# Performance work log

Hardware: AMD Instinct MI355X
Metric: run time of the kernel (lower is better)

The kernel has to match this reference:

```python
import jax, jax.numpy as jnp
import numpy as np

_EPS = 1e-5

def _ln(x, scale, shift):
    # Faithful to the module's custom layer norm: variance term is the SUM of
    # squared deviations over the feature dim (not the mean), and the affine is
    # scale * normed + shift with scale=b*, shift=s* (argument order as in source).
    m = jnp.mean(x, axis=-1, keepdims=True)
    d = x - m
    ssq = jnp.sum(d * d, axis=-1, keepdims=True)
    return scale * (d / jnp.sqrt(ssq + _EPS)) + shift


def setup_inputs() -> dict:
    key = jax.random.key(0)
    ks = jax.random.split(key, 12)
    B, T, I, H = 64, 512, 512, 512
    f32 = jnp.float32
    return {
        "x": jax.random.normal(ks[0], (B, T, I), f32),
        "hx": jax.random.normal(ks[1], (B, H), f32),
        "cx": jax.random.normal(ks[2], (B, H), f32),
        "Wi": jax.random.normal(ks[3], (4 * H, I), f32) / np.float32(np.sqrt(I)),
        "Wh": jax.random.normal(ks[4], (4 * H, H), f32) / np.float32(np.sqrt(H)),
        "bias": jax.random.normal(ks[5], (4 * H,), f32) * 0.1,
        "b1": jax.random.normal(ks[6], (4 * H,), f32) * 0.1,
        "b2": jax.random.normal(ks[7], (4 * H,), f32) * 0.1,
        "b3": jax.random.normal(ks[8], (H,), f32) * 0.1,
        "s1": 1.0 + jax.random.normal(ks[9], (4 * H,), f32) * 0.1,
        "s2": 1.0 + jax.random.normal(ks[10], (4 * H,), f32) * 0.1,
        "s3": 1.0 + jax.random.normal(ks[11], (H,), f32) * 0.1,
    }


def reference(x, hx, cx, Wi, Wh, bias, b1, b2, b3, s1, s2, s3):
    # x: [B, T, I] (batch_first). Work in time-major for the scan.
    xT = jnp.swapaxes(x, 0, 1)  # [T, B, I]
    # The input-projection layer norm has no cross-time dependency -> precompute.
    gi = _ln(jnp.einsum('tbi,gi->tbg', xT, Wi), b1, s1)  # [T, B, 4H]

    def step(carry, gi_t):
        h, c = carry
        gates = gi_t + _ln(h @ Wh.T, b2, s2) + bias  # [B, 4H]
        i, f, g, o = jnp.split(gates, 4, axis=-1)
        i = jax.nn.sigmoid(i)
        f = jax.nn.sigmoid(f)
        g = jnp.tanh(g)
        o = jax.nn.sigmoid(o)
        c_new = _ln(f * c + i * g, b3, s3)
        h_new = o * jnp.tanh(c_new)
        return (h_new, c_new), h_new

    (hy, cy), ys = jax.lax.scan(step, (hx, cx), gi)
    output = jnp.swapaxes(ys, 0, 1)  # back to [B, T, H]
    return output, hy, cy
```

## Files before the change

kernel.cpp:

```cpp
#include <hip/hip_runtime.h>
#include <cstdint>
#include <cstddef>


typedef float  f32x4 __attribute__((ext_vector_type(4)));
typedef __bf16 bf16x8 __attribute__((ext_vector_type(8)));
typedef unsigned int u32x4 __attribute__((ext_vector_type(4)));
typedef unsigned short u16x4 __attribute__((ext_vector_type(4)));

#define DEV __device__ __forceinline__

#define LD4_AGENT(dst, p) asm volatile("global_load_dwordx4 %0, %1, off sc1" : "=v"(dst) : "v"(p))
#define VM0_FENCE() do{ asm volatile("s_waitcnt vmcnt(0)" ::: "memory"); \
                        __builtin_amdgcn_sched_barrier(0); }while(0)

DEV unsigned short f2b(float f){
  unsigned int u = __builtin_bit_cast(unsigned int, f);
  unsigned int r = (u + 0x7FFFu + ((u >> 16) & 1u)) >> 16;
  return (unsigned short)r;
}
DEV float b2f(unsigned short s){
  unsigned int u = ((unsigned int)s) << 16;
  return __builtin_bit_cast(float, u);
}
DEV float tanh_fast(float x){
  const float e = __expf(2.f * x);
  return 1.f - 2.f * __builtin_amdgcn_rcpf(e + 1.f);
}
DEV float sigmoid_fast(float x){
  return __builtin_amdgcn_rcpf(1.f + __expf(-x));
}

__global__ __launch_bounds__(256) void conv_bf16(const float* __restrict__ src,
                                                 unsigned short* __restrict__ dst,
                                                 int n4){
  int i = blockIdx.x * 256 + threadIdx.x;
  if (i >= n4) return;
  f32x4 v = ((const f32x4*)src)[i];
  u16x4 o;
  #pragma unroll
  for (int j = 0; j < 4; ++j) o[j] = f2b(v[j]);
  ((u16x4*)dst)[i] = o;
}

__global__ __launch_bounds__(256, 2) void gemm_gi(const unsigned short* __restrict__ Xb,
                                                  const unsigned short* __restrict__ Wib,
                                                  unsigned short* __restrict__ Gp){
  __shared__ unsigned short As[128 * 48];
  __shared__ unsigned short Bs[128 * 48];
  const int tid = threadIdx.x;
  const int m0 = blockIdx.x * 128;
  const int n0 = blockIdx.y * 128;
  const int w = tid >> 6, lane = tid & 63;
  const int lr = lane & 15, lq = lane >> 4;
  const int wm = (w & 1) * 64, wn = (w >> 1) * 64;
  const int sr = tid >> 2;
  const int sc = (tid & 3) * 8;
  const unsigned short* gx = Xb + (size_t)(m0 + sr) * 512 + sc;
  const unsigned short* gw = Wib + (size_t)(n0 + sr) * 512 + sc;
  f32x4 acc[4][4] = {};
  for (int kb = 0; kb < 16; ++kb){
    u32x4 a0 = *(const u32x4*)(gx + kb * 32);
    u32x4 a1 = *(const u32x4*)(gx + 64 * 512 + kb * 32);
    u32x4 b0 = *(const u32x4*)(gw + kb * 32);
    u32x4 b1 = *(const u32x4*)(gw + 64 * 512 + kb * 32);
    __syncthreads();
    *(u32x4*)&As[sr * 48 + sc] = a0;
    *(u32x4*)&As[(sr + 64) * 48 + sc] = a1;
    *(u32x4*)&Bs[sr * 48 + sc] = b0;
    *(u32x4*)&Bs[(sr + 64) * 48 + sc] = b1;
    __syncthreads();
    bf16x8 af[4], bfv[4];
    #pragma unroll
    for (int mi = 0; mi < 4; ++mi) af[mi] = *(const bf16x8*)&As[(wm + mi * 16 + lr) * 48 + lq * 8];
    #pragma unroll
    for (int ni = 0; ni < 4; ++ni) bfv[ni] = *(const bf16x8*)&Bs[(wn + ni * 16 + lr) * 48 + lq * 8];
    #pragma unroll
    for (int mi = 0; mi < 4; ++mi)
      #pragma unroll
      for (int ni = 0; ni < 4; ++ni)
        acc[mi][ni] = __builtin_amdgcn_mfma_f32_16x16x32_bf16(af[mi], bfv[ni], acc[mi][ni], 0, 0, 0);
  }
  #pragma unroll
  for (int mi = 0; mi < 4; ++mi){
    const int rowb = m0 + wm + mi * 16 + lq * 4;
    #pragma unroll
    for (int ni = 0; ni < 4; ++ni){
      const int col = n0 + wn + ni * 16 + lr;
      #pragma unroll
      for (int r = 0; r < 4; ++r)
        Gp[(size_t)(rowb + r) * 2048 + col] = f2b(acc[mi][ni][r]);
    }
  }
}

__global__ __launch_bounds__(256) void ln_rows(unsigned short* __restrict__ G,
                                               const float* __restrict__ b1,
                                               const float* __restrict__ s1){
  const int row = blockIdx.x;
  const int tid = threadIdx.x;
  unsigned short* rp = G + (size_t)row * 2048 + tid * 8;
  u32x4 raw = *(const u32x4*)rp;
  float x[8];
  #pragma unroll
  for (int j = 0; j < 8; ++j){
    unsigned int word = raw[j >> 1];
    unsigned short us = (j & 1) ? (unsigned short)(word >> 16) : (unsigned short)(word & 0xFFFF);
    x[j] = b2f(us);
  }
  float s = 0.f, q = 0.f;
  #pragma unroll
  for (int j = 0; j < 8; ++j){ s += x[j]; q += x[j] * x[j]; }
  #pragma unroll
  for (int o = 1; o < 64; o <<= 1){ s += __shfl_xor(s, o); q += __shfl_xor(q, o); }
  __shared__ float ps[4][2];
  const int wv = tid >> 6;
  if ((tid & 63) == 0){ ps[wv][0] = s; ps[wv][1] = q; }
  __syncthreads();
  s = ps[0][0] + ps[1][0] + ps[2][0] + ps[3][0];
  q = ps[0][1] + ps[1][1] + ps[2][1] + ps[3][1];
  const float mu = s * (1.f / 2048.f);
  const float inv = rsqrtf((q - s * mu) + 1e-5f);
  const float* b1p = b1 + tid * 8;
  const float* s1p = s1 + tid * 8;
  u32x4 outw;
  #pragma unroll
  for (int j = 0; j < 4; ++j){
    float y0 = b1p[2 * j]     * ((x[2 * j]     - mu) * inv) + s1p[2 * j];
    float y1 = b1p[2 * j + 1] * ((x[2 * j + 1] - mu) * inv) + s1p[2 * j + 1];
    outw[j] = (unsigned int)f2b(y0) | ((unsigned int)f2b(y1) << 16);
  }
  *(u32x4*)rp = outw;
}

__global__ __launch_bounds__(512, 2) void lstm_rec(
    const unsigned short* __restrict__ Gi,
    const unsigned short* __restrict__ Whb,
    const float* __restrict__ bias,
    const float* __restrict__ b2, const float* __restrict__ s2,
    const float* __restrict__ b3, const float* __restrict__ s3,
    const float* __restrict__ hx,
    const float* __restrict__ cx,
    unsigned int* __restrict__ hbuf,
    unsigned long long* __restrict__ pF,
    unsigned long long* __restrict__ pA,
    unsigned long long* __restrict__ pCs,
    float* __restrict__ out){
  const int tid = threadIdx.x;
  const int tm = (blockIdx.x >> 1) & 3;
  const int ks = ((blockIdx.x >> 3) << 1) | (blockIdx.x & 1);
  const int w = tid >> 6;
  const int lane = tid & 63;
  const int lr = lane & 15, lq = lane >> 4;

  const int type = w >> 1;
  const int jloc = (w & 1) * 16 + lr;
  const int row_g = type * 512 + ks * 32 + jloc;
  const float b2r = b2[row_g];
  const float sbr = s2[row_g] + bias[row_g];

  bf16x8 bfr[16];
  {
    const unsigned short* wr = Whb + (size_t)row_g * 512 + lq * 8;
    #pragma unroll
    for (int kk = 0; kk < 16; ++kk) bfr[kk] = *(const bf16x8*)(wr + kk * 32);
  }

  const int cs = tid >> 5;
  const int cj = tid & 31;
  const int hcol = ks * 32 + cj;
  const int bidx = tm * 16 + cs;
  float c_val = cx[(size_t)bidx * 512 + hcol];
  const float b3j = b3[hcol], s3j = s3[hcol];

  const int psmp = 2 * w + (lane >> 5);
  const int pidx = lane & 31;
  const int pl_slice = (lane >> 1) & 15;
  const int pl_kind  = lane & 1;

  float b3c[16], s3c[16];
  #pragma unroll
  for (int q = 0; q < 4; ++q)
    #pragma unroll
    for (int j = 0; j < 4; ++j){
      const int c = 4 * pidx + 128 * q + j;
      b3c[4 * q + j] = b3[c];
      s3c[4 * q + j] = s3[c];
    }

  __shared__ unsigned short hlds[16 * 520];
  __shared__ float act[4][32][17];
  __shared__ float redA[8][16][2];
  __shared__ float stAl[16][2];

  float cc_own = 0.f, o_own = 0.f;

  for (int t = 0; t < 512; ++t){
    float giv[4];
    #pragma unroll
    for (int r = 0; r < 4; ++r){
      const int b = tm * 16 + lq * 4 + r;
      giv[r] = b2f(Gi[((size_t)b * 512 + t) * 2048 + row_g]);
    }

    if (t == 0){
      const float* hr = hx + (size_t)(tm * 16 + psmp) * 512;
      #pragma unroll
      for (int q = 0; q < 4; ++q){
        f32x4 hv4 = *(const f32x4*)(hr + 4 * pidx + 128 * q);
        unsigned long long pk = 0;
        #pragma unroll
        for (int j = 0; j < 4; ++j)
          pk |= (unsigned long long)f2b(hv4[j]) << (16 * j);
        *(unsigned long long*)&hlds[psmp * 520 + 4 * pidx + 128 * q] = pk;
      }
    } else {
      const unsigned int tg = (unsigned)t;
      const unsigned long long* fp = pF + (size_t)(t & 1) * 64 + tm * 16 + (lane & 15);
      const unsigned long long* sp =
          pCs + ((size_t)(t & 1) * 4 + tm) * 512 + pl_slice * 32 + psmp * 2 + pl_kind;
      unsigned long long sv;
      for (;;){
        unsigned long long fv = __hip_atomic_load(fp, __ATOMIC_RELAXED, __HIP_MEMORY_SCOPE_AGENT);
        sv = __hip_atomic_load(sp, __ATOMIC_RELAXED, __HIP_MEMORY_SCOPE_AGENT);
        bool ok = ((unsigned)fv == tg) & ((unsigned)(sv >> 32) == tg);
        if (__all((int)ok)) break;
        __builtin_amdgcn_s_sleep(1);
      }
      const unsigned int* hsrc =
          hbuf + (size_t)(t & 1) * 32768 + (size_t)(tm * 16 + psmp) * 512;
      u32x4 pay[4];
      #pragma unroll
      for (int q = 0; q < 4; ++q) LD4_AGENT(pay[q], hsrc + 4 * pidx + 128 * q);
      float pv = __builtin_bit_cast(float, (unsigned)sv);
      #pragma unroll
      for (int o = 2; o < 32; o <<= 1) pv += __shfl_xor(pv, o);
      const float ov = __shfl_xor(pv, 1);
      const float S = pl_kind ? ov : pv;
      const float Q = pl_kind ? pv : ov;
      const float mu = S * (1.f / 512.f);
      const float inv = rsqrtf((Q - S * mu) + 1e-5f);
      c_val = b3j * ((cc_own - mu) * inv) + s3j;
      const float h_self = o_own * tanh_fast(c_val);
      out[((size_t)bidx * 512 + (t - 1)) * 512 + hcol] = h_self;
      VM0_FENCE();
      #pragma unroll
      for (int q = 0; q < 4; ++q){
        unsigned long long pk = 0;
        #pragma unroll
        for (int j = 0; j < 4; ++j){
          const unsigned int v = pay[q][j];
          const float ccv = b2f((unsigned short)(v & 0xFFFF));
          const float oov = b2f((unsigned short)(v >> 16));
          const float h = oov * tanh_fast(b3c[4 * q + j] * ((ccv - mu) * inv) + s3c[4 * q + j]);
          pk |= (unsigned long long)f2b(h) << (16 * j);
        }
        *(unsigned long long*)&hlds[psmp * 520 + 4 * pidx + 128 * q] = pk;
      }
    }
    __syncthreads();

    f32x4 acc = {0.f, 0.f, 0.f, 0.f};
    #pragma unroll
    for (int kk = 0; kk < 16; ++kk){
      bf16x8 af = *(const bf16x8*)&hlds[lr * 520 + lq * 8 + kk * 32];
      acc = __builtin_amdgcn_mfma_f32_16x16x32_bf16(af, bfr[kk], acc, 0, 0, 0);
    }
    #pragma unroll
    for (int r = 0; r < 4; ++r){
      float s = acc[r], q = acc[r] * acc[r];
      #pragma unroll
      for (int o = 1; o < 16; o <<= 1){ s += __shfl_xor(s, o); q += __shfl_xor(q, o); }
      if (lr == 0){ redA[w][lq * 4 + r][0] = s; redA[w][lq * 4 + r][1] = q; }
    }
    __syncthreads();

    unsigned long long* slotA = pA + ((size_t)(t & 1) * 4 + tm) * 512;
    const unsigned int atag = (unsigned)(t + 1);
    if (w == 0 && lane < 32){
      const int smp = lane >> 1, kd = lane & 1;
      float Sp = 0.f;
      #pragma unroll
      for (int w2 = 0; w2 < 8; ++w2) Sp += redA[w2][smp][kd];
      const unsigned long long pvs = ((unsigned long long)atag << 32) |
          (unsigned long long)__builtin_bit_cast(unsigned int, Sp);
      __hip_atomic_store(slotA + (size_t)ks * 32 + lane, pvs,
                         __ATOMIC_RELAXED, __HIP_MEMORY_SCOPE_AGENT);
    }
    {
      const unsigned long long* ap = slotA + pl_slice * 32 + psmp * 2 + pl_kind;
      unsigned long long av;
      for (;;){
        av = __hip_atomic_load(ap, __ATOMIC_RELAXED, __HIP_MEMORY_SCOPE_AGENT);
        if (__all((int)((unsigned)(av >> 32) == atag))) break;
        __builtin_amdgcn_s_sleep(2);
      }
      float pv = __builtin_bit_cast(float, (unsigned)av);
      #pragma unroll
      for (int o = 2; o < 32; o <<= 1) pv += __shfl_xor(pv, o);
      const float ov = __shfl_xor(pv, 1);
      const float S = pl_kind ? ov : pv;
      const float Q = pl_kind ? pv : ov;
      if ((lane & 31) == 0){
        const float mu = S * (1.f / 2048.f);
        stAl[psmp][0] = mu;
        stAl[psmp][1] = rsqrtf((Q - S * mu) + 1e-5f);
      }
    }
    __syncthreads();

    #pragma unroll
    for (int r = 0; r < 4; ++r){
      const int s0 = lq * 4 + r;
      const float nv = (acc[r] - stAl[s0][0]) * stAl[s0][1];
      const float gv = giv[r] + b2r * nv + sbr;
      float a;
      if (type == 2) a = tanh_fast(gv);
      else           a = sigmoid_fast(gv);
      act[type][jloc][s0] = a;
    }
    __syncthreads();

    const float i_g = act[0][cj][cs];
    const float f_g = act[1][cj][cs];
    const float g_g = act[2][cj][cs];
    const float o_g = act[3][cj][cs];
    const float cc = f_g * c_val + i_g * g_g;
    const unsigned int ntag = (unsigned)(t + 1);
    const size_t np = (size_t)((t + 1) & 1);
    {
      const unsigned int pv32 = (unsigned int)f2b(cc) | ((unsigned int)f2b(o_g) << 16);
      __hip_atomic_store(hbuf + np * 32768 + (size_t)bidx * 512 + hcol, pv32,
                         __ATOMIC_RELAXED, __HIP_MEMORY_SCOPE_AGENT);
    }
    float sC = cc, qC = cc * cc;
    #pragma unroll
    for (int o = 1; o < 32; o <<= 1){ sC += __shfl_xor(sC, o); qC += __shfl_xor(qC, o); }
    unsigned long long* slotC = pCs + (np * 4 + tm) * 512;
    if ((lane & 31) < 2){
      const float v = (lane & 1) ? qC : sC;
      const unsigned long long pvs = ((unsigned long long)ntag << 32) |
          (unsigned long long)__builtin_bit_cast(unsigned int, v);
      __hip_atomic_store(slotC + (size_t)ks * 32 + cs * 2 + (lane & 1), pvs,
                         __ATOMIC_RELAXED, __HIP_MEMORY_SCOPE_AGENT);
    }
    VM0_FENCE();
    __syncthreads();
    if (tid == 0)
      __hip_atomic_store(pF + np * 64 + tm * 16 + ks, (unsigned long long)ntag,
                         __ATOMIC_RELAXED, __HIP_MEMORY_SCOPE_AGENT);
    cc_own = cc; o_own = o_g;
  }

  {
    const unsigned long long* sp =
        pCs + ((size_t)0 * 4 + tm) * 512 + pl_slice * 32 + psmp * 2 + pl_kind;
    unsigned long long sv;
    for (;;){
      sv = __hip_atomic_load(sp, __ATOMIC_RELAXED, __HIP_MEMORY_SCOPE_AGENT);
      if (__all((int)((unsigned)(sv >> 32) == 512u))) break;
      __builtin_amdgcn_s_sleep(2);
    }
    float pv = __builtin_bit_cast(float, (unsigned)sv);
    #pragma unroll
    for (int o = 2; o < 32; o <<= 1) pv += __shfl_xor(pv, o);
    const float ov = __shfl_xor(pv, 1);
    const float S = pl_kind ? ov : pv;
    const float Q = pl_kind ? pv : ov;
    const float mu = S * (1.f / 512.f);
    const float inv = rsqrtf((Q - S * mu) + 1e-5f);
    const float cn = b3j * ((cc_own - mu) * inv) + s3j;
    const float h = o_own * tanh_fast(cn);
    out[((size_t)bidx * 512 + 511) * 512 + hcol] = h;
    out[16777216u + (size_t)bidx * 512 + hcol] = h;
    out[16777216u + 32768u + (size_t)bidx * 512 + hcol] = cn;
  }
}

extern "C" void kernel_launch(void* const* d_in, const int* in_sizes, int n_in,
                              void* d_out, int out_size, void* d_ws, size_t ws_size,
                              hipStream_t stream){
  (void)in_sizes; (void)n_in; (void)out_size; (void)ws_size;
  const float* x    = (const float*)d_in[0];
  const float* hx   = (const float*)d_in[1];
  const float* cx   = (const float*)d_in[2];
  const float* Wi   = (const float*)d_in[3];
  const float* Wh   = (const float*)d_in[4];
  const float* bias = (const float*)d_in[5];
  const float* b1   = (const float*)d_in[6];
  const float* b2   = (const float*)d_in[7];
  const float* b3   = (const float*)d_in[8];
  const float* s1   = (const float*)d_in[9];
  const float* s2   = (const float*)d_in[10];
  const float* s3   = (const float*)d_in[11];
  float* out = (float*)d_out;
  char* ws = (char*)d_ws;

  unsigned short*     xb   = (unsigned short*)(ws);
  unsigned short*     wib  = (unsigned short*)(ws + 33554432);
  unsigned short*     whb  = (unsigned short*)(ws + 35651584);
  unsigned short*     gp   = (unsigned short*)(ws + 37748736);
  unsigned int*       hbuf = (unsigned int*)(ws + 171966464);
  unsigned long long* pF   = (unsigned long long*)(ws + 172228608);
  unsigned long long* pA   = (unsigned long long*)(ws + 172490752);
  unsigned long long* pCs  = (unsigned long long*)(ws + 172523520);

  hipMemsetAsync(pF, 0, 327680, stream);
  conv_bf16<<<16384, 256, 0, stream>>>(x,  xb,  4194304);
  conv_bf16<<<1024,  256, 0, stream>>>(Wi, wib, 262144);
  conv_bf16<<<1024,  256, 0, stream>>>(Wh, whb, 262144);
  gemm_gi<<<dim3(256, 16, 1), 256, 0, stream>>>(xb, wib, gp);
  ln_rows<<<32768, 256, 0, stream>>>(gp, b1, s1);
  lstm_rec<<<64, 512, 0, stream>>>(gp, whb, bias, b2, s2, b3, s3, hx, cx,
                                   hbuf, pF, pA, pCs, out);
}
```

Before: 3.245 ms.

## Tag each h payload with step counter, removing per-block flag barrier

Each hidden-state payload now carries its timestep tag in the upper 32 bits of a 64-bit word. Consumers spin on the tagged payload itself and re-poll until every loaded element matches, instead of waiting on a separate per-block flag. This removes the producer's vmcnt fence, a __syncthreads, and the flag store at the end of each step, shortening the serial critical path. In exchange the hidden-state buffer is twice as large, so more bytes are read per step, and consumers may spin more often on partially arrived data.

Measured after the change: 3.265 ms. Within noise of the previous version (+0.6%).

```diff
diff --git a/kernel.cpp b/kernel.cpp
--- a/kernel.cpp
+++ b/kernel.cpp
@@ -141,8 +141,7 @@
     const float* __restrict__ b3, const float* __restrict__ s3,
     const float* __restrict__ hx,
     const float* __restrict__ cx,
-    unsigned int* __restrict__ hbuf,
-    unsigned long long* __restrict__ pF,
+    unsigned long long* __restrict__ hbuf,
     unsigned long long* __restrict__ pA,
     unsigned long long* __restrict__ pCs,
     float* __restrict__ out){
@@ -180,13 +179,11 @@
 
   float b3c[16], s3c[16];
   #pragma unroll
-  for (int q = 0; q < 4; ++q)
-    #pragma unroll
-    for (int j = 0; j < 4; ++j){
-      const int c = 4 * pidx + 128 * q + j;
-      b3c[4 * q + j] = b3[c];
-      s3c[4 * q + j] = s3[c];
-    }
+  for (int q = 0; q < 8; ++q){
+    const int c0 = 2 * pidx + 64 * q;
+    b3c[2 * q]     = b3[c0];     b3c[2 * q + 1] = b3[c0 + 1];
+    s3c[2 * q]     = s3[c0];     s3c[2 * q + 1] = s3[c0 + 1];
+  }
 
   __shared__ unsigned short hlds[16 * 520];
   __shared__ float act[4][32][17];
@@ -216,22 +213,22 @@
       }
     } else {
       const unsigned int tg = (unsigned)t;
-      const unsigned long long* fp = pF + (size_t)(t & 1) * 64 + tm * 16 + (lane & 15);
+      const unsigned long long* hbase =
+          hbuf + (size_t)(t & 1) * 32768 + (size_t)(tm * 16 + psmp) * 512;
+      const unsigned long long* hpre = hbase + pl_slice * 32 + pl_kind * 16;
       const unsigned long long* sp =
           pCs + ((size_t)(t & 1) * 4 + tm) * 512 + pl_slice * 32 + psmp * 2 + pl_kind;
       unsigned long long sv;
       for (;;){
-        unsigned long long fv = __hip_atomic_load(fp, __ATOMIC_RELAXED, __HIP_MEMORY_SCOPE_AGENT);
+        unsigned long long pv = __hip_atomic_load(hpre, __ATOMIC_RELAXED, __HIP_MEMORY_SCOPE_AGENT);
         sv = __hip_atomic_load(sp, __ATOMIC_RELAXED, __HIP_MEMORY_SCOPE_AGENT);
-        bool ok = ((unsigned)fv == tg) & ((unsigned)(sv >> 32) == tg);
+        bool ok = ((unsigned)(pv >> 32) == tg) & ((unsigned)(sv >> 32) == tg);
         if (__all((int)ok)) break;
         __builtin_amdgcn_s_sleep(1);
       }
-      const unsigned int* hsrc =
-          hbuf + (size_t)(t & 1) * 32768 + (size_t)(tm * 16 + psmp) * 512;
-      u32x4 pay[4];
-      #pragma unroll
-      for (int q = 0; q < 4; ++q) LD4_AGENT(pay[q], hsrc + 4 * pidx + 128 * q);
+      u32x4 pay[8];
+      #pragma unroll
+      for (int q = 0; q < 8; ++q) LD4_AGENT(pay[q], hbase + 2 * pidx + 64 * q);
       float pv = __builtin_bit_cast(float, (unsigned)sv);
       #pragma unroll
       for (int o = 2; o < 32; o <<= 1) pv += __shfl_xor(pv, o);
@@ -244,18 +241,27 @@
       const float h_self = o_own * tanh_fast(c_val);
       out[((size_t)bidx * 512 + (t - 1)) * 512 + hcol] = h_self;
       VM0_FENCE();
-      #pragma unroll
-      for (int q = 0; q < 4; ++q){
-        unsigned long long pk = 0;
+      for (;;){
+        bool ok = true;
         #pragma unroll
-        for (int j = 0; j < 4; ++j){
-          const unsigned int v = pay[q][j];
-          const float ccv = b2f((unsigned short)(v & 0xFFFF));
-          const float oov = b2f((unsigned short)(v >> 16));
-          const float h = oov * tanh_fast(b3c[4 * q + j] * ((ccv - mu) * inv) + s3c[4 * q + j]);
-          pk |= (unsigned long long)f2b(h) << (16 * j);
-        }
-        *(unsigned long long*)&hlds[psmp * 520 + 4 * pidx + 128 * q] = pk;
+        for (int q = 0; q < 8; ++q) ok &= (pay[q][1] == tg) & (pay[q][3] == tg);
+        if (__all((int)ok)) break;
+        __builtin_amdgcn_s_sleep(1);
+        #pragma unroll
+        for (int q = 0; q < 8; ++q) LD4_AGENT(pay[q], hbase + 2 * pidx + 64 * q);
+        VM0_FENCE();
+      }
+      #pragma unroll
+      for (int q = 0; q < 8; ++q){
+        const unsigned int v0 = pay[q][0], v1 = pay[q][2];
+        const float cc0 = b2f((unsigned short)(v0 & 0xFFFF));
+        const float oo0 = b2f((unsigned short)(v0 >> 16));
+        const float cc1 = b2f((unsigned short)(v1 & 0xFFFF));
+        const float oo1 = b2f((unsigned short)(v1 >> 16));
+        const float h0 = oo0 * tanh_fast(b3c[2 * q]     * ((cc0 - mu) * inv) + s3c[2 * q]);
+        const float h1 = oo1 * tanh_fast(b3c[2 * q + 1] * ((cc1 - mu) * inv) + s3c[2 * q + 1]);
+        *(unsigned int*)&hlds[psmp * 520 + 2 * pidx + 64 * q] =
+            (unsigned)f2b(h0) | ((unsigned)f2b(h1) << 16);
       }
     }
     __syncthreads();
@@ -329,8 +335,9 @@
     const unsigned int ntag = (unsigned)(t + 1);
     const size_t np = (size_t)((t + 1) & 1);
     {
-      const unsigned int pv32 = (unsigned int)f2b(cc) | ((unsigned int)f2b(o_g) << 16);
-      __hip_atomic_store(hbuf + np * 32768 + (size_t)bidx * 512 + hcol, pv32,
+      const unsigned long long pvh = ((unsigned long long)ntag << 32) |
+          (unsigned long long)f2b(cc) | ((unsigned long long)f2b(o_g) << 16);
+      __hip_atomic_store(hbuf + np * 32768 + (size_t)bidx * 512 + hcol, pvh,
                          __ATOMIC_RELAXED, __HIP_MEMORY_SCOPE_AGENT);
     }
     float sC = cc, qC = cc * cc;
@@ -344,11 +351,6 @@
       __hip_atomic_store(slotC + (size_t)ks * 32 + cs * 2 + (lane & 1), pvs,
                          __ATOMIC_RELAXED, __HIP_MEMORY_SCOPE_AGENT);
     }
-    VM0_FENCE();
-    __syncthreads();
-    if (tid == 0)
-      __hip_atomic_store(pF + np * 64 + tm * 16 + ks, (unsigned long long)ntag,
-                         __ATOMIC_RELAXED, __HIP_MEMORY_SCOPE_AGENT);
     cc_own = cc; o_own = o_g;
   }
 
@@ -400,17 +402,16 @@
   unsigned short*     wib  = (unsigned short*)(ws + 33554432);
   unsigned short*     whb  = (unsigned short*)(ws + 35651584);
   unsigned short*     gp   = (unsigned short*)(ws + 37748736);
-  unsigned int*       hbuf = (unsigned int*)(ws + 171966464);
-  unsigned long long* pF   = (unsigned long long*)(ws + 172228608);
+  unsigned long long* hbuf = (unsigned long long*)(ws + 171966464);
   unsigned long long* pA   = (unsigned long long*)(ws + 172490752);
   unsigned long long* pCs  = (unsigned long long*)(ws + 172523520);
 
-  hipMemsetAsync(pF, 0, 327680, stream);
+  hipMemsetAsync(hbuf, 0, 589824, stream);
   conv_bf16<<<16384, 256, 0, stream>>>(x,  xb,  4194304);
   conv_bf16<<<1024,  256, 0, stream>>>(Wi, wib, 262144);
   conv_bf16<<<1024,  256, 0, stream>>>(Wh, whb, 262144);
   gemm_gi<<<dim3(256, 16, 1), 256, 0, stream>>>(xb, wib, gp);
   ln_rows<<<32768, 256, 0, stream>>>(gp, b1, s1);
   lstm_rec<<<64, 512, 0, stream>>>(gp, whb, bias, b2, s2, b3, s3, hx, cx,
-                                   hbuf, pF, pA, pCs, out);
-}
+                                   hbuf, pA, pCs, out);
+}
```
